# Performance work log

Measured on AMD Instinct MI355X. Metric: run time of the kernel, lower is better.

Reference implementation:

```python
import jax, jax.numpy as jnp
import numpy as np

N_DST = 50000
N_SRC = 50000
E = 800000
D = 128
R = 3
H_SEM = 128
NEG_SLOPE = 0.2  # DGL GATConv default


def setup_inputs() -> dict:
    key = jax.random.key(0)
    ks = jax.random.split(key, 40)
    s = 1.0 / np.sqrt(D)
    inp = {
        'dst_feat': jax.random.normal(ks[0], (N_DST, D), jnp.float32),
        'src_feat0': jax.random.normal(ks[1], (N_SRC, D), jnp.float32),
        'src_feat1': jax.random.normal(ks[2], (N_SRC, D), jnp.float32),
        'src_feat2': jax.random.normal(ks[3], (N_SRC, D), jnp.float32),
        'sem_W1': jax.random.normal(ks[4], (D, H_SEM), jnp.float32) * s,
        'sem_b1': jnp.zeros((H_SEM,), jnp.float32),
        'sem_W2': jax.random.normal(ks[5], (H_SEM, 1), jnp.float32) * (1.0 / np.sqrt(H_SEM)),
    }
    for r in range(R):
        inp[f'Wg{r}'] = jax.random.normal(ks[6 + r], (D, D), jnp.float32) * s
        inp[f'al{r}'] = jax.random.normal(ks[9 + r], (D,), jnp.float32) * s
        inp[f'ar{r}'] = jax.random.normal(ks[12 + r], (D,), jnp.float32) * s
        inp[f'bg{r}'] = jnp.zeros((D,), jnp.float32)
        inp[f'src_idx{r}'] = jax.random.randint(ks[15 + r], (E,), 0, N_SRC, jnp.int32)
        inp[f'dst_idx{r}'] = jax.random.randint(ks[18 + r], (E,), 0, N_DST, jnp.int32)
    return inp


def _gat(fs, fd, W, al, ar, b, sidx, didx):
    # DGL GATConv, num_heads=1, bipartite, eval mode (no dropout)
    hs = fs @ W                    # [Ns, D]
    hd = fd @ W                    # [Nd, D]
    el = hs @ al                   # [Ns]
    er = hd @ ar                   # [Nd]
    e = jax.nn.leaky_relu(el[sidx] + er[didx], NEG_SLOPE)  # [E]
    # edge softmax over incoming edges of each dst node
    m = jax.ops.segment_max(e, didx, num_segments=N_DST)
    a = jnp.exp(e - m[didx])
    z = jax.ops.segment_sum(a, didx, num_segments=N_DST)
    alpha = a / z[didx]            # [E]
    out = jax.ops.segment_sum(hs[sidx] * alpha[:, None], didx, num_segments=N_DST)
    return jax.nn.elu(out + b)     # [Nd, D]


def reference(dst_feat, src_feat0, src_feat1, src_feat2,
              Wg0, Wg1, Wg2, al0, al1, al2, ar0, ar1, ar2, bg0, bg1, bg2,
              sem_W1, sem_b1, sem_W2,
              src_idx0, src_idx1, src_idx2, dst_idx0, dst_idx1, dst_idx2):
    z0 = _gat(src_feat0, dst_feat, Wg0, al0, ar0, bg0, src_idx0, dst_idx0)
    z1 = _gat(src_feat1, dst_feat, Wg1, al1, ar1, bg1, src_idx1, dst_idx1)
    z2 = _gat(src_feat2, dst_feat, Wg2, al2, ar2, bg2, src_idx2, dst_idx2)
    z_m = jnp.stack([z0, z1, z2], axis=1)            # [N, R, D]
    h = jnp.tanh(z_m @ sem_W1 + sem_b1) @ sem_W2     # [N, R, 1]
    w = h.mean(axis=0)                               # [R, 1]
    a_w = jax.nn.softmax(w, axis=0)                  # [R, 1]
    z = (z_m * a_w[None, :, :]).sum(axis=1)          # [N, D]
    att_mp = a_w.squeeze()                           # [R]
    return (z, att_mp)
```

## Files before the change

kernel.cpp:

```cpp
#include <hip/hip_runtime.h>
#include <math.h>

#define D_DIM 128
#define N_DST 50000
#define N_SRC 50000
#define NE    800000
#define NEG_SLOPE 0.2f

#define NB        196
#define CAP       4608
#define CHUNK     8192
#define NBLK_REL  98
#define GEMM_BLKS 196
#define GEMM_GRID (3 * GEMM_BLKS)
#define ER_PB     86

typedef unsigned short ushort_t;
using f32x4  = __attribute__((ext_vector_type(4))) float;
using bf16x8 = __attribute__((ext_vector_type(8))) short;

__device__ __forceinline__ ushort_t f2bf(float x) {
    unsigned u = __float_as_uint(x);
    unsigned r = (u + 0x7fffu + ((u >> 16) & 1u)) >> 16;
    return (ushort_t)r;
}
__device__ __forceinline__ float bf2f(ushort_t b) {
    return __uint_as_float(((unsigned)b) << 16);
}
__device__ __forceinline__ float bflo(unsigned u) { return __uint_as_float(u << 16); }
__device__ __forceinline__ float bfhi(unsigned u) { return __uint_as_float(u & 0xffff0000u); }
__device__ __forceinline__ float tanh_fast(float x) {
    float e = __expf(2.f * x);
    return 1.f - 2.f / (e + 1.f);
}

__device__ __forceinline__ void cvt8(float4 f0, float4 f1, bf16x8& hi, bf16x8& lo) {
    float f[8] = {f0.x, f0.y, f0.z, f0.w, f1.x, f1.y, f1.z, f1.w};
    #pragma unroll
    for (int i = 0; i < 8; i++) {
        ushort_t h = f2bf(f[i]);
        hi[i] = (short)h;
        lo[i] = (short)(ushort_t)(__float_as_uint(f[i] - bf2f(h)) >> 16);
    }
}

__global__ __launch_bounds__(256) void vecprep_kernel(
        const float* __restrict__ Wg0, const float* __restrict__ Wg1,
        const float* __restrict__ Wg2,
        const float* __restrict__ ar0, const float* __restrict__ ar1,
        const float* __restrict__ ar2,
        const float* __restrict__ W1,
        float* __restrict__ wv, ushort_t* __restrict__ Wt_g,
        ushort_t* __restrict__ Bv) {
    int bx = blockIdx.x, tid = threadIdx.x;
    if (bx < 3) {
        if (tid < 128) {
            const float* W  = bx == 0 ? Wg0 : (bx == 1 ? Wg1 : Wg2);
            const float* ar = bx == 0 ? ar0 : (bx == 1 ? ar1 : ar2);
            float sar = 0.f;
            for (int j = 0; j < D_DIM; j++) sar = fmaf(W[tid * D_DIM + j], ar[j], sar);
            wv[bx * D_DIM + tid] = sar;
        }
    } else if (bx < 67) {
        int idx = (bx - 3) * 256 + tid;
        int k = idx >> 7, n = idx & 127;
        Wt_g[n * 128 + k] = f2bf(W1[idx]);
    } else {
        int q = bx - 67;
        int rel = q >> 6;
        int idx = (q & 63) * 256 + tid;
        const float* W = rel == 0 ? Wg0 : (rel == 1 ? Wg1 : Wg2);
        int k = idx >> 7, n = idx & 127;
        float v = W[idx];
        ushort_t hi = f2bf(v);
        ushort_t lo = f2bf(v - bf2f(hi));
        int nt = n >> 4, l15 = n & 15;
        int kc = k >> 5, quad = (k >> 3) & 3, e = k & 7;
        int h2 = nt >> 2, n4 = nt & 3;
        int lane = quad * 16 + l15;
        int fh = kc * 16 + h2 * 8 + n4;
        ushort_t* dst = Bv + (size_t)rel * 32768;
        dst[(fh)     * 512 + lane * 8 + e] = hi;
        dst[(fh + 4) * 512 + lane * 8 + e] = lo;
    }
}

__global__ __launch_bounds__(256) void bucket_scatter_kernel(
        const int* __restrict__ d0, const int* __restrict__ d1, const int* __restrict__ d2,
        const int* __restrict__ s0, const int* __restrict__ s1, const int* __restrict__ s2,
        int* __restrict__ bucketCur, int2* __restrict__ pairs) {
    __shared__ int cnt[NB], base[NB], cur[NB];
    int bx = blockIdx.x;
    int r = bx / NBLK_REL, blk = bx % NBLK_REL;
    const int* dd = r == 0 ? d0 : (r == 1 ? d1 : d2);
    const int* ss = r == 0 ? s0 : (r == 1 ? s1 : s2);
    int tid = threadIdx.x;
    if (tid < NB) { cnt[tid] = 0; cur[tid] = 0; }
    __syncthreads();
    int e0 = blk * CHUNK, e1 = min(e0 + CHUNK, NE);
    for (int e = e0 + tid; e < e1; e += 256) atomicAdd(&cnt[dd[e] >> 8], 1);
    __syncthreads();
    if (tid < NB) base[tid] = cnt[tid] ? atomicAdd(&bucketCur[r * NB + tid], cnt[tid]) : 0;
    __syncthreads();
    for (int e = e0 + tid; e < e1; e += 256) {
        int d = dd[e], b = d >> 8;
        int rank = atomicAdd(&cur[b], 1);
        pairs[(size_t)(r * NB + b) * CAP + base[b] + rank] = make_int2(ss[e], d);
    }
}

__global__ __launch_bounds__(256) void csr_kernel(
        const int2* __restrict__ pairs, const int* __restrict__ bucketCur,
        int* __restrict__ offs, int* __restrict__ cnts, int* __restrict__ perm) {
    __shared__ int hist[256], sc[256], cur[256];
    int bx = blockIdx.x;
    int r = bx / NB, b = bx % NB;
    int tid = threadIdx.x;
    int nE = bucketCur[r * NB + b];
    size_t region = (size_t)(r * NB + b) * CAP;
    const int2* pr = pairs + region;
    hist[tid] = 0;
    __syncthreads();
    for (int i = tid; i < nE; i += 256) atomicAdd(&hist[pr[i].y & 255], 1);
    __syncthreads();
    int v = hist[tid];
    sc[tid] = v;
    __syncthreads();
    for (int off = 1; off < 256; off <<= 1) {
        int t = tid >= off ? sc[tid - off] : 0;
        __syncthreads();
        sc[tid] += t;
        __syncthreads();
    }
    int excl = sc[tid] - v;
    int dstg = b * 256 + tid;
    if (dstg < N_DST) { offs[r * N_DST + dstg] = (int)region + excl; cnts[r * N_DST + dstg] = v; }
    cur[tid] = excl;
    __syncthreads();
    int* pm = perm + region;
    for (int i = tid; i < nE; i += 256) {
        int2 p = pr[i];
        int rank = atomicAdd(&cur[p.y & 255], 1);
        pm[rank] = p.x;
    }
}

__global__ __launch_bounds__(512) void gemm_er_kernel(
        const float* __restrict__ A0, const float* __restrict__ A1, const float* __restrict__ A2,
        const ushort_t* __restrict__ Bv,
        const float* __restrict__ al0, const float* __restrict__ al1, const float* __restrict__ al2,
        const float* __restrict__ dstf, const float* __restrict__ wv,
        ushort_t* __restrict__ hs, float* __restrict__ elv) {
    __shared__ ushort_t Bs[32768];
    int bx = blockIdx.x;
    int rel = bx / GEMM_BLKS, blk = bx % GEMM_BLKS;
    const float* A  = rel == 0 ? A0 : (rel == 1 ? A1 : A2);
    const float* al = rel == 0 ? al0 : (rel == 1 ? al1 : al2);
    ushort_t* C = hs + (size_t)rel * N_SRC * 128;
    int tid = threadIdx.x;

    {
        const uint4* src = (const uint4*)(Bv + (size_t)rel * 32768);
        uint4* dl = (uint4*)Bs;
        #pragma unroll
        for (int i = 0; i < 8; i++) dl[tid + i * 512] = src[tid + i * 512];
    }

    int w = tid >> 6, lane = tid & 63;
    int quad = lane >> 4, l15 = lane & 15;
    int row0 = blk * 256 + w * 32;

    int gr0 = row0 + l15;      if (gr0 > N_SRC - 1) gr0 = N_SRC - 1;
    int gr1 = row0 + 16 + l15; if (gr1 > N_SRC - 1) gr1 = N_SRC - 1;
    const float* a0p = A + (size_t)gr0 * 128 + quad * 8;
    const float* a1p = A + (size_t)gr1 * 128 + quad * 8;

    float4 abuf[2][2][2];
    abuf[0][0][0] = *(const float4*)(a0p + 0);
    abuf[0][0][1] = *(const float4*)(a0p + 4);
    abuf[0][1][0] = *(const float4*)(a1p + 0);
    abuf[0][1][1] = *(const float4*)(a1p + 4);

    __syncthreads();

    f32x4 acc[2][8] = {};
    #pragma unroll
    for (int kc = 0; kc < 4; kc++) {
        const int par = kc & 1;
        if (kc < 3) {
            int ko = (kc + 1) * 32;
            abuf[par ^ 1][0][0] = *(const float4*)(a0p + ko);
            abuf[par ^ 1][0][1] = *(const float4*)(a0p + ko + 4);
            abuf[par ^ 1][1][0] = *(const float4*)(a1p + ko);
            abuf[par ^ 1][1][1] = *(const float4*)(a1p + ko + 4);
        }
        bf16x8 ah[2], alo[2];
        #pragma unroll
        for (int t = 0; t < 2; t++)
            cvt8(abuf[par][t][0], abuf[par][t][1], ah[t], alo[t]);

        #pragma unroll
        for (int h2 = 0; h2 < 2; h2++) {
            #pragma unroll
            for (int n4 = 0; n4 < 4; n4++) {
                int f = kc * 16 + h2 * 8 + n4;
                bf16x8 bh = *(const bf16x8*)&Bs[f * 512 + lane * 8];
                bf16x8 bl = *(const bf16x8*)&Bs[(f + 4) * 512 + lane * 8];
                int nt = h2 * 4 + n4;
                #pragma unroll
                for (int t = 0; t < 2; t++) {
                    acc[t][nt] = __builtin_amdgcn_mfma_f32_16x16x32_bf16(ah[t],  bh, acc[t][nt], 0, 0, 0);
                    acc[t][nt] = __builtin_amdgcn_mfma_f32_16x16x32_bf16(alo[t], bh, acc[t][nt], 0, 0, 0);
                    acc[t][nt] = __builtin_amdgcn_mfma_f32_16x16x32_bf16(ah[t],  bl, acc[t][nt], 0, 0, 0);
                }
            }
        }
    }

    float alv[8];
    #pragma unroll
    for (int nt = 0; nt < 8; nt++) alv[nt] = al[nt * 16 + l15];
    #pragma unroll
    for (int t = 0; t < 2; t++) {
        float part[4] = {0.f, 0.f, 0.f, 0.f};
        #pragma unroll
        for (int nt = 0; nt < 8; nt++)
            #pragma unroll
            for (int i = 0; i < 4; i++)
                part[i] = fmaf(acc[t][nt][i], alv[nt], part[i]);
        #pragma unroll
        for (int msk = 1; msk < 16; msk <<= 1)
            #pragma unroll
            for (int i = 0; i < 4; i++) part[i] += __shfl_xor(part[i], msk);
        if (l15 == 0) {
            #pragma unroll
            for (int i = 0; i < 4; i++) {
                int gr = row0 + t * 16 + quad * 4 + i;
                if (gr < N_SRC) elv[rel * N_DST + gr] = part[i];
            }
        }
    }

    int erbase = bx * ER_PB;
    float m0[11], m1[11];
    float wl0 = 0.f, wh0 = 0.f, wl1 = 0.f, wh1 = 0.f, wl2 = 0.f, wh2 = 0.f;
    int rend = 0;
    if (erbase < N_DST) {
        rend = min(erbase + ER_PB, N_DST);
        wl0 = wv[lane];       wh0 = wv[lane + 64];
        wl1 = wv[128 + lane]; wh1 = wv[128 + lane + 64];
        wl2 = wv[256 + lane]; wh2 = wv[256 + lane + 64];
        #pragma unroll
        for (int j = 0; j < 11; j++) {
            int r = erbase + w + 8 * j;
            int rr = r < rend ? r : erbase;
            m0[j] = dstf[(size_t)rr * 128 + lane];
            m1[j] = dstf[(size_t)rr * 128 + lane + 64];
        }
    }

    __syncthreads();

    ushort_t* Csh = Bs + w * 2304;
    #pragma unroll
    for (int h = 0; h < 2; h++) {
        __asm__ __volatile__("" ::: "memory");
        #pragma unroll
        for (int t = 0; t < 2; t++)
            #pragma unroll
            for (int ntl = 0; ntl < 4; ntl++) {
                int nt = h * 4 + ntl;
                #pragma unroll
                for (int i = 0; i < 4; i++)
                    Csh[(t * 16 + quad * 4 + i) * 72 + ntl * 16 + l15] = f2bf(acc[t][nt][i]);
            }
        __asm__ __volatile__("" ::: "memory");
        int r2 = lane >> 1, cb = (lane & 1) * 32;
        int gr = row0 + r2;
        if (gr < N_SRC) {
            ushort_t* dst = C + (size_t)gr * 128 + h * 64 + cb;
            #pragma unroll
            for (int k2 = 0; k2 < 4; k2++) {
                uint4 v = *(const uint4*)&Csh[r2 * 72 + cb + k2 * 8];
                *(uint4*)(dst + k2 * 8) = v;
            }
        }
    }

    if (erbase < N_DST) {
        #pragma unroll
        for (int j = 0; j < 11; j++) {
            int r = erbase + w + 8 * j;
            if (r < rend) {
                float p0 = fmaf(m0[j], wl0, m1[j] * wh0);
                float p1 = fmaf(m0[j], wl1, m1[j] * wh1);
                float p2 = fmaf(m0[j], wl2, m1[j] * wh2);
                #pragma unroll
                for (int off = 32; off > 0; off >>= 1) {
                    p0 += __shfl_down(p0, off);
                    p1 += __shfl_down(p1, off);
                    p2 += __shfl_down(p2, off);
                }
                if (lane == 0) {
                    elv[3 * N_DST + r] = p0;
                    elv[4 * N_DST + r] = p1;
                    elv[5 * N_DST + r] = p2;
                }
            }
        }
    }
}

__global__ __launch_bounds__(256) void aggregate_kernel(
        const ushort_t* __restrict__ hs, const float* __restrict__ elv,
        const int* __restrict__ perm, const int* __restrict__ offs,
        const int* __restrict__ cnts,
        const float* __restrict__ bg0, const float* __restrict__ bg1,
        const float* __restrict__ bg2, float* __restrict__ zm) {
    __shared__ int2 ew[4][128];
    int wave = threadIdx.x >> 6, lane = threadIdx.x & 63;
    int bx  = blockIdx.x;
    int rel = bx / 12500;
    int b   = (bx % 12500) * 4 + wave;
    const float* el  = elv + rel * N_DST;
    float erb = elv[(3 + rel) * N_DST + b];
    const float* bg = rel == 0 ? bg0 : (rel == 1 ? bg1 : bg2);
    const ushort_t* hsr = hs + (size_t)rel * N_SRC * 128;
    int o0 = offs[rel * N_DST + b], deg = cnts[rel * N_DST + b];
    float* zout = zm + ((size_t)b * 3 + rel) * 128;

    if (deg <= 128) {
        int s0 = 0, s1 = 0;
        float e0 = 0.f, e1 = 0.f;
        if (deg <= 64) {
            if (lane < deg) {
                s0 = perm[o0 + lane];
                float x = el[s0] + erb;
                x = x >= 0.f ? x : NEG_SLOPE * x;
                e0 = __expf(x);
            }
        } else {
            int i0 = lane, i1 = lane + 64;
            float x0 = -INFINITY, x1 = -INFINITY;
            if (i0 < deg) { s0 = perm[o0 + i0]; float x = el[s0] + erb; x0 = x >= 0.f ? x : NEG_SLOPE * x; }
            if (i1 < deg) { s1 = perm[o0 + i1]; float x = el[s1] + erb; x1 = x >= 0.f ? x : NEG_SLOPE * x; }
            float m = fmaxf(x0, x1);
            #pragma unroll
            for (int msk = 1; msk < 64; msk <<= 1) m = fmaxf(m, __shfl_xor(m, msk));
            e0 = (i0 < deg) ? __expf(x0 - m) : 0.f;
            e1 = (i1 < deg) ? __expf(x1 - m) : 0.f;
        }
        float lsum = e0 + e1;
        #pragma unroll
        for (int msk = 1; msk < 64; msk <<= 1) lsum += __shfl_xor(lsum, msk);
        float invz = deg > 0 ? 1.f / lsum : 0.f;

        ew[wave][lane] = make_int2(s0 * 256, __float_as_int(e0 * invz));
        if (deg > 64)
            ew[wave][lane + 64] = make_int2(s1 * 256, __float_as_int(e1 * invz));
        __asm__ __volatile__("" ::: "memory");

        int degp = (deg + 7) & ~7;
        const char* base = (const char*)hsr;
        int half = lane >> 5;
        int col8 = (lane & 31) * 8;
        float2 a01 = {0.f, 0.f}, a23 = {0.f, 0.f};
        for (int j = 0; j < degp; j += 8) {
            int2 pA = ew[wave][j + half];
            int2 pB = ew[wave][j + 2 + half];
            int2 pC = ew[wave][j + 4 + half];
            int2 pD = ew[wave][j + 6 + half];
            uint2 hA = *(const uint2*)(base + (unsigned)(pA.x + col8));
            uint2 hB = *(const uint2*)(base + (unsigned)(pB.x + col8));
            uint2 hC = *(const uint2*)(base + (unsigned)(pC.x + col8));
            uint2 hD = *(const uint2*)(base + (unsigned)(pD.x + col8));
            float eA = __int_as_float(pA.y), eB = __int_as_float(pB.y);
            float eC = __int_as_float(pC.y), eD = __int_as_float(pD.y);
            a01.x = fmaf(eA, bflo(hA.x), a01.x); a01.y = fmaf(eA, bfhi(hA.x), a01.y);
            a23.x = fmaf(eA, bflo(hA.y), a23.x); a23.y = fmaf(eA, bfhi(hA.y), a23.y);
            a01.x = fmaf(eB, bflo(hB.x), a01.x); a01.y = fmaf(eB, bfhi(hB.x), a01.y);
            a23.x = fmaf(eB, bflo(hB.y), a23.x); a23.y = fmaf(eB, bfhi(hB.y), a23.y);
            a01.x = fmaf(eC, bflo(hC.x), a01.x); a01.y = fmaf(eC, bfhi(hC.x), a01.y);
            a23.x = fmaf(eC, bflo(hC.y), a23.x); a23.y = fmaf(eC, bfhi(hC.y), a23.y);
            a01.x = fmaf(eD, bflo(hD.x), a01.x); a01.y = fmaf(eD, bfhi(hD.x), a01.y);
            a23.x = fmaf(eD, bflo(hD.y), a23.x); a23.y = fmaf(eD, bfhi(hD.y), a23.y);
        }
        a01.x += __shfl_xor(a01.x, 32);
        a01.y += __shfl_xor(a01.y, 32);
        a23.x += __shfl_xor(a23.x, 32);
        a23.y += __shfl_xor(a23.y, 32);
        if (half == 0) {
            int col4 = (lane & 31) * 4;
            float4 bgv = *(const float4*)&bg[col4];
            float4 z;
            z.x = a01.x + bgv.x;
            z.y = a01.y + bgv.y;
            z.z = a23.x + bgv.z;
            z.w = a23.y + bgv.w;
            z.x = z.x > 0.f ? z.x : __expf(z.x) - 1.f;
            z.y = z.y > 0.f ? z.y : __expf(z.y) - 1.f;
            z.z = z.z > 0.f ? z.z : __expf(z.z) - 1.f;
            z.w = z.w > 0.f ? z.w : __expf(z.w) - 1.f;
            *(float4*)&zout[col4] = z;
        }
    } else {
        float lmax = -INFINITY;
        for (int i = lane; i < deg; i += 64) {
            int s = perm[o0 + i];
            float x = el[s] + erb;
            x = x >= 0.f ? x : NEG_SLOPE * x;
            lmax = fmaxf(lmax, x);
        }
        #pragma unroll
        for (int msk = 1; msk < 64; msk <<= 1) lmax = fmaxf(lmax, __shfl_xor(lmax, msk));
        float lsum = 0.f;
        for (int i = lane; i < deg; i += 64) {
            int s = perm[o0 + i];
            float x = el[s] + erb;
            x = x >= 0.f ? x : NEG_SLOPE * x;
            lsum += __expf(x - lmax);
        }
        #pragma unroll
        for (int msk = 1; msk < 64; msk <<= 1) lsum += __shfl_xor(lsum, msk);
        float invz = 1.f / lsum;
        float c0 = 0.f, c1 = 0.f;
        int col2 = lane * 2;
        for (int j = 0; j < deg; j++) {
            int s = perm[o0 + j];
            float x = el[s] + erb;
            x = x >= 0.f ? x : NEG_SLOPE * x;
            float e_ = __expf(x - lmax) * invz;
            unsigned hv = *(const unsigned*)(hsr + (size_t)s * 128 + col2);
            c0 = fmaf(e_, bflo(hv), c0);
            c1 = fmaf(e_, bfhi(hv), c1);
        }
        float2 z;
        z.x = c0 + bg[col2];
        z.y = c1 + bg[col2 + 1];
        z.x = z.x > 0.f ? z.x : __expf(z.x) - 1.f;
        z.y = z.y > 0.f ? z.y : __expf(z.y) - 1.f;
        *(float2*)&zout[col2] = z;
    }
}

__global__ __launch_bounds__(256) void semantic_kernel(
        const float* __restrict__ zm, const ushort_t* __restrict__ Wt_g,
        const float* __restrict__ b1, const float* __restrict__ W2,
        float* __restrict__ w_sum) {
    __shared__ ushort_t Wt[128 * 136];
    __shared__ float hsum[3];
    const int NROWS = N_DST * 3;
    int tid = threadIdx.x;
    if (tid < 3) hsum[tid] = 0.f;

    #pragma unroll
    for (int i = 0; i < 8; i++) {
        int c = i * 256 + tid;
        int n = c >> 4, c16 = c & 15;
        uint4 t = *(const uint4*)(Wt_g + n * 128 + c16 * 8);
        *(uint4*)&Wt[n * 136 + c16 * 8] = t;
    }
    __syncthreads();

    int w    = tid >> 6, lane = tid & 63;
    int quad = lane >> 4, l15 = lane & 15;
    long row0 = (long)blockIdx.x * 64 + w * 16;
    long rA = row0 + l15; if (rA > NROWS - 1) rA = NROWS - 1;

    f32x4 acc[8] = {};
    #pragma unroll
    for (int kc = 0; kc < 4; kc++) {
        int k0 = kc * 32 + quad * 8;
        const float* src = zm + (size_t)rA * 128 + k0;
        float4 f0 = *(const float4*)src;
        float4 f1 = *(const float4*)(src + 4);
        bf16x8 a;
        a[0] = (short)f2bf(f0.x); a[1] = (short)f2bf(f0.y);
        a[2] = (short)f2bf(f0.z); a[3] = (short)f2bf(f0.w);
        a[4] = (short)f2bf(f1.x); a[5] = (short)f2bf(f1.y);
        a[6] = (short)f2bf(f1.z); a[7] = (short)f2bf(f1.w);
        #pragma unroll
        for (int nt = 0; nt < 8; nt++) {
            int n = nt * 16 + l15;
            bf16x8 bfr = *(const bf16x8*)&Wt[n * 136 + k0];
            acc[nt] = __builtin_amdgcn_mfma_f32_16x16x32_bf16(a, bfr, acc[nt], 0, 0, 0);
        }
    }

    float part[4] = {0.f, 0.f, 0.f, 0.f};
    #pragma unroll
    for (int nt = 0; nt < 8; nt++) {
        int n = nt * 16 + l15;
        float bb = b1[n], ww = W2[n];
        #pragma unroll
        for (int i = 0; i < 4; i++) {
            float t = tanh_fast(acc[nt][i] + bb);
            part[i] = fmaf(t, ww, part[i]);
        }
    }
    #pragma unroll
    for (int msk = 1; msk < 16; msk <<= 1)
        #pragma unroll
        for (int i = 0; i < 4; i++) part[i] += __shfl_xor(part[i], msk);
    if (l15 == 0) {
        #pragma unroll
        for (int i = 0; i < 4; i++) {
            long R = row0 + quad * 4 + i;
            if (R < NROWS) atomicAdd(&hsum[(int)(R % 3)], part[i]);
        }
    }
    __syncthreads();
    if (tid < 3) atomicAdd(&w_sum[tid], hsum[tid]);
}

__global__ void combine_kernel(const float* __restrict__ zm, const float* __restrict__ w_sum,
                               float* __restrict__ out, float* __restrict__ out_att) {
    float w0 = w_sum[0] * (1.f / (float)N_DST);
    float w1 = w_sum[1] * (1.f / (float)N_DST);
    float w2 = w_sum[2] * (1.f / (float)N_DST);
    float m = fmaxf(w0, fmaxf(w1, w2));
    float e0 = __expf(w0 - m), e1 = __expf(w1 - m), e2 = __expf(w2 - m);
    float s = 1.f / (e0 + e1 + e2);
    float a0 = e0 * s, a1 = e1 * s, a2 = e2 * s;
    if (blockIdx.x == 0 && threadIdx.x < 3)
        out_att[threadIdx.x] = threadIdx.x == 0 ? a0 : (threadIdx.x == 1 ? a1 : a2);
    int id4 = blockIdx.x * 256 + threadIdx.x;
    int n  = id4 >> 5;
    int d4 = (id4 & 31) * 4;
    const float4 z0 = *(const float4*)&zm[((size_t)n * 3 + 0) * 128 + d4];
    const float4 z1 = *(const float4*)&zm[((size_t)n * 3 + 1) * 128 + d4];
    const float4 z2 = *(const float4*)&zm[((size_t)n * 3 + 2) * 128 + d4];
    float4 o;
    o.x = a0 * z0.x + a1 * z1.x + a2 * z2.x;
    o.y = a0 * z0.y + a1 * z1.y + a2 * z2.y;
    o.z = a0 * z0.z + a1 * z1.z + a2 * z2.z;
    o.w = a0 * z0.w + a1 * z1.w + a2 * z2.w;
    *(float4*)&out[(size_t)n * 128 + d4] = o;
}

extern "C" void kernel_launch(void* const* d_in, const int* in_sizes, int n_in,
                              void* d_out, int out_size, void* d_ws, size_t ws_size,
                              hipStream_t stream) {
    const float* dstf   = (const float*)d_in[0];
    const float* src0   = (const float*)d_in[1];
    const float* src1   = (const float*)d_in[2];
    const float* src2   = (const float*)d_in[3];
    const float* sem_W1 = (const float*)d_in[4];
    const float* sem_b1 = (const float*)d_in[5];
    const float* sem_W2 = (const float*)d_in[6];
    const float* Wg[3]  = {(const float*)d_in[7],  (const float*)d_in[13], (const float*)d_in[19]};
    const float* al[3]  = {(const float*)d_in[8],  (const float*)d_in[14], (const float*)d_in[20]};
    const float* ar[3]  = {(const float*)d_in[9],  (const float*)d_in[15], (const float*)d_in[21]};
    const float* bg[3]  = {(const float*)d_in[10], (const float*)d_in[16], (const float*)d_in[22]};
    const int*  sidx[3] = {(const int*)d_in[11], (const int*)d_in[17], (const int*)d_in[23]};
    const int*  didx[3] = {(const int*)d_in[12], (const int*)d_in[18], (const int*)d_in[24]};
    float* out = (float*)d_out;

    char* p = (char*)d_ws;
    auto alloc = [&](size_t bytes) -> char* {
        char* q = p; p += (bytes + 255) & ~(size_t)255; return q;
    };
    float*    zm   = (float*)alloc((size_t)N_DST * 3 * 128 * 4);
    ushort_t* hs   = (ushort_t*)alloc((size_t)3 * N_SRC * 128 * 2);
    float*    elv  = (float*)alloc((size_t)6 * N_DST * 4);
    float*    wv   = (float*)alloc((size_t)3 * 128 * 4);
    ushort_t* Wt_g = (ushort_t*)alloc((size_t)128 * 128 * 2);
    ushort_t* Bv   = (ushort_t*)alloc((size_t)3 * 32768 * 2);
    int* cnts = (int*)alloc((size_t)3 * N_DST * 4);
    int* offs = (int*)alloc((size_t)3 * N_DST * 4);
    int* perm = (int*)alloc((size_t)3 * NB * CAP * 4);
    int* zero = (int*)alloc((size_t)(3 * NB + 8) * 4);
    int*   bucketCur = zero;
    float* wsum      = (float*)(zero + 3 * NB);
    int2* pairs = (int2*)zm;

    hipMemsetAsync(zero, 0, (size_t)(3 * NB + 8) * 4, stream);

    vecprep_kernel<<<259, 256, 0, stream>>>(Wg[0], Wg[1], Wg[2], ar[0], ar[1], ar[2],
                                            sem_W1, wv, Wt_g, Bv);
    bucket_scatter_kernel<<<3 * NBLK_REL, 256, 0, stream>>>(didx[0], didx[1], didx[2],
                                                            sidx[0], sidx[1], sidx[2],
                                                            bucketCur, pairs);
    csr_kernel<<<3 * NB, 256, 0, stream>>>(pairs, bucketCur, offs, cnts, perm);
    gemm_er_kernel<<<GEMM_GRID, 512, 0, stream>>>(src0, src1, src2, Bv,
                                                  al[0], al[1], al[2],
                                                  dstf, wv, hs, elv);
    aggregate_kernel<<<3 * 12500, 256, 0, stream>>>(hs, elv, perm, offs, cnts,
                                                    bg[0], bg[1], bg[2], zm);
    semantic_kernel<<<(3 * N_DST + 63) / 64, 256, 0, stream>>>(zm, Wt_g, sem_b1, sem_W2, wsum);
    combine_kernel<<<6250, 256, 0, stream>>>(zm, wsum, out, out + (size_t)N_DST * 128);
}
```

Measured before the change: 435.4 us.

## Map one half-wave per destination node in aggregation; persistent-grid semantic kernel

The aggregation kernel now gives each destination node 32 lanes instead of a full 64-lane wave, so each block covers 8 nodes and the grid is halved. Each lane loads 16-byte bf16 chunks and keeps 8 accumulators, and the fast path now covers degrees up to 64 instead of 128; higher degrees fall to the slow serial path. This targets idle lanes on the typical degree of about 16 and improves gather width. The semantic kernel becomes a grid-stride loop over 512 blocks, which cuts the number of per-block shared-memory and global atomic flushes but leaves fewer blocks to hide latency.

```diff
diff --git a/kernel.cpp b/kernel.cpp
--- a/kernel.cpp
+++ b/kernel.cpp
@@ -14,6 +14,8 @@
 #define GEMM_BLKS 196
 #define GEMM_GRID (3 * GEMM_BLKS)
 #define ER_PB     86
+#define SEM_GRID  512
+#define SEM_TILES ((3 * N_DST + 63) / 64)
 
 typedef unsigned short ushort_t;
 using f32x4  = __attribute__((ext_vector_type(4))) float;
@@ -317,129 +319,133 @@
         const int* __restrict__ cnts,
         const float* __restrict__ bg0, const float* __restrict__ bg1,
         const float* __restrict__ bg2, float* __restrict__ zm) {
-    __shared__ int2 ew[4][128];
-    int wave = threadIdx.x >> 6, lane = threadIdx.x & 63;
+    __shared__ int2 ew[4][2][64];
+    int tid = threadIdx.x;
+    int wave = tid >> 6, lane = tid & 63;
+    int hw = lane >> 5, l31 = lane & 31;
     int bx  = blockIdx.x;
-    int rel = bx / 12500;
-    int b   = (bx % 12500) * 4 + wave;
+    int rel = bx / 6250;
+    int b   = (bx % 6250) * 8 + wave * 2 + hw;
     const float* el  = elv + rel * N_DST;
     float erb = elv[(3 + rel) * N_DST + b];
     const float* bg = rel == 0 ? bg0 : (rel == 1 ? bg1 : bg2);
     const ushort_t* hsr = hs + (size_t)rel * N_SRC * 128;
     int o0 = offs[rel * N_DST + b], deg = cnts[rel * N_DST + b];
     float* zout = zm + ((size_t)b * 3 + rel) * 128;
-
-    if (deg <= 128) {
+    int2* ews = ew[wave][hw];
+
+    if (deg <= 64) {
         int s0 = 0, s1 = 0;
         float e0 = 0.f, e1 = 0.f;
-        if (deg <= 64) {
-            if (lane < deg) {
-                s0 = perm[o0 + lane];
-                float x = el[s0] + erb;
-                x = x >= 0.f ? x : NEG_SLOPE * x;
-                e0 = __expf(x);
-            }
-        } else {
-            int i0 = lane, i1 = lane + 64;
-            float x0 = -INFINITY, x1 = -INFINITY;
-            if (i0 < deg) { s0 = perm[o0 + i0]; float x = el[s0] + erb; x0 = x >= 0.f ? x : NEG_SLOPE * x; }
-            if (i1 < deg) { s1 = perm[o0 + i1]; float x = el[s1] + erb; x1 = x >= 0.f ? x : NEG_SLOPE * x; }
-            float m = fmaxf(x0, x1);
-            #pragma unroll
-            for (int msk = 1; msk < 64; msk <<= 1) m = fmaxf(m, __shfl_xor(m, msk));
-            e0 = (i0 < deg) ? __expf(x0 - m) : 0.f;
-            e1 = (i1 < deg) ? __expf(x1 - m) : 0.f;
+        if (l31 < deg) {
+            s0 = perm[o0 + l31];
+            float x = el[s0] + erb;
+            x = x >= 0.f ? x : NEG_SLOPE * x;
+            e0 = __expf(x);
+        }
+        if (deg > 32 && l31 + 32 < deg) {
+            s1 = perm[o0 + l31 + 32];
+            float x = el[s1] + erb;
+            x = x >= 0.f ? x : NEG_SLOPE * x;
+            e1 = __expf(x);
         }
         float lsum = e0 + e1;
         #pragma unroll
-        for (int msk = 1; msk < 64; msk <<= 1) lsum += __shfl_xor(lsum, msk);
+        for (int msk = 1; msk < 32; msk <<= 1) lsum += __shfl_xor(lsum, msk);
         float invz = deg > 0 ? 1.f / lsum : 0.f;
 
-        ew[wave][lane] = make_int2(s0 * 256, __float_as_int(e0 * invz));
-        if (deg > 64)
-            ew[wave][lane + 64] = make_int2(s1 * 256, __float_as_int(e1 * invz));
+        ews[l31] = make_int2(s0 * 256, __float_as_int(e0 * invz));
+        if (deg > 32)
+            ews[l31 + 32] = make_int2(s1 * 256, __float_as_int(e1 * invz));
         __asm__ __volatile__("" ::: "memory");
 
-        int degp = (deg + 7) & ~7;
-        const char* base = (const char*)hsr;
-        int half = lane >> 5;
-        int col8 = (lane & 31) * 8;
-        float2 a01 = {0.f, 0.f}, a23 = {0.f, 0.f};
-        for (int j = 0; j < degp; j += 8) {
-            int2 pA = ew[wave][j + half];
-            int2 pB = ew[wave][j + 2 + half];
-            int2 pC = ew[wave][j + 4 + half];
-            int2 pD = ew[wave][j + 6 + half];
-            uint2 hA = *(const uint2*)(base + (unsigned)(pA.x + col8));
-            uint2 hB = *(const uint2*)(base + (unsigned)(pB.x + col8));
-            uint2 hC = *(const uint2*)(base + (unsigned)(pC.x + col8));
-            uint2 hD = *(const uint2*)(base + (unsigned)(pD.x + col8));
+        int degp = (deg + 3) & ~3;
+        const char* basep = (const char*)hsr;
+        int sub = l31 >> 4;
+        int col16 = (l31 & 15) * 16;
+        float a0 = 0.f, a1 = 0.f, a2 = 0.f, a3 = 0.f;
+        float a4 = 0.f, a5 = 0.f, a6 = 0.f, a7 = 0.f;
+        for (int j = 0; j < degp; j += 4) {
+            int2 pA = ews[j + sub];
+            int2 pB = ews[j + 2 + sub];
+            uint4 hA = *(const uint4*)(basep + (unsigned)(pA.x + col16));
+            uint4 hB = *(const uint4*)(basep + (unsigned)(pB.x + col16));
             float eA = __int_as_float(pA.y), eB = __int_as_float(pB.y);
-            float eC = __int_as_float(pC.y), eD = __int_as_float(pD.y);
-            a01.x = fmaf(eA, bflo(hA.x), a01.x); a01.y = fmaf(eA, bfhi(hA.x), a01.y);
-            a23.x = fmaf(eA, bflo(hA.y), a23.x); a23.y = fmaf(eA, bfhi(hA.y), a23.y);
-            a01.x = fmaf(eB, bflo(hB.x), a01.x); a01.y = fmaf(eB, bfhi(hB.x), a01.y);
-            a23.x = fmaf(eB, bflo(hB.y), a23.x); a23.y = fmaf(eB, bfhi(hB.y), a23.y);
-            a01.x = fmaf(eC, bflo(hC.x), a01.x); a01.y = fmaf(eC, bfhi(hC.x), a01.y);
-            a23.x = fmaf(eC, bflo(hC.y), a23.x); a23.y = fmaf(eC, bfhi(hC.y), a23.y);
-            a01.x = fmaf(eD, bflo(hD.x), a01.x); a01.y = fmaf(eD, bfhi(hD.x), a01.y);
-            a23.x = fmaf(eD, bflo(hD.y), a23.x); a23.y = fmaf(eD, bfhi(hD.y), a23.y);
-        }
-        a01.x += __shfl_xor(a01.x, 32);
-        a01.y += __shfl_xor(a01.y, 32);
-        a23.x += __shfl_xor(a23.x, 32);
-        a23.y += __shfl_xor(a23.y, 32);
-        if (half == 0) {
-            int col4 = (lane & 31) * 4;
-            float4 bgv = *(const float4*)&bg[col4];
-            float4 z;
-            z.x = a01.x + bgv.x;
-            z.y = a01.y + bgv.y;
-            z.z = a23.x + bgv.z;
-            z.w = a23.y + bgv.w;
-            z.x = z.x > 0.f ? z.x : __expf(z.x) - 1.f;
-            z.y = z.y > 0.f ? z.y : __expf(z.y) - 1.f;
-            z.z = z.z > 0.f ? z.z : __expf(z.z) - 1.f;
-            z.w = z.w > 0.f ? z.w : __expf(z.w) - 1.f;
-            *(float4*)&zout[col4] = z;
+            a0 = fmaf(eA, bflo(hA.x), a0); a1 = fmaf(eA, bfhi(hA.x), a1);
+            a2 = fmaf(eA, bflo(hA.y), a2); a3 = fmaf(eA, bfhi(hA.y), a3);
+            a4 = fmaf(eA, bflo(hA.z), a4); a5 = fmaf(eA, bfhi(hA.z), a5);
+            a6 = fmaf(eA, bflo(hA.w), a6); a7 = fmaf(eA, bfhi(hA.w), a7);
+            a0 = fmaf(eB, bflo(hB.x), a0); a1 = fmaf(eB, bfhi(hB.x), a1);
+            a2 = fmaf(eB, bflo(hB.y), a2); a3 = fmaf(eB, bfhi(hB.y), a3);
+            a4 = fmaf(eB, bflo(hB.z), a4); a5 = fmaf(eB, bfhi(hB.z), a5);
+            a6 = fmaf(eB, bflo(hB.w), a6); a7 = fmaf(eB, bfhi(hB.w), a7);
+        }
+        a0 += __shfl_xor(a0, 16); a1 += __shfl_xor(a1, 16);
+        a2 += __shfl_xor(a2, 16); a3 += __shfl_xor(a3, 16);
+        a4 += __shfl_xor(a4, 16); a5 += __shfl_xor(a5, 16);
+        a6 += __shfl_xor(a6, 16); a7 += __shfl_xor(a7, 16);
+        if (sub == 0) {
+            int c = (l31 & 15) * 8;
+            float4 bgv0 = *(const float4*)&bg[c];
+            float4 bgv1 = *(const float4*)&bg[c + 4];
+            float4 z0, z1;
+            z0.x = a0 + bgv0.x; z0.y = a1 + bgv0.y;
+            z0.z = a2 + bgv0.z; z0.w = a3 + bgv0.w;
+            z1.x = a4 + bgv1.x; z1.y = a5 + bgv1.y;
+            z1.z = a6 + bgv1.z; z1.w = a7 + bgv1.w;
+            z0.x = z0.x > 0.f ? z0.x : __expf(z0.x) - 1.f;
+            z0.y = z0.y > 0.f ? z0.y : __expf(z0.y) - 1.f;
+            z0.z = z0.z > 0.f ? z0.z : __expf(z0.z) - 1.f;
+            z0.w = z0.w > 0.f ? z0.w : __expf(z0.w) - 1.f;
+            z1.x = z1.x > 0.f ? z1.x : __expf(z1.x) - 1.f;
+            z1.y = z1.y > 0.f ? z1.y : __expf(z1.y) - 1.f;
+            z1.z = z1.z > 0.f ? z1.z : __expf(z1.z) - 1.f;
+            z1.w = z1.w > 0.f ? z1.w : __expf(z1.w) - 1.f;
+            *(float4*)&zout[c] = z0;
+            *(float4*)&zout[c + 4] = z1;
         }
     } else {
         float lmax = -INFINITY;
-        for (int i = lane; i < deg; i += 64) {
+        for (int i = l31; i < deg; i += 32) {
             int s = perm[o0 + i];
             float x = el[s] + erb;
             x = x >= 0.f ? x : NEG_SLOPE * x;
             lmax = fmaxf(lmax, x);
         }
         #pragma unroll
-        for (int msk = 1; msk < 64; msk <<= 1) lmax = fmaxf(lmax, __shfl_xor(lmax, msk));
+        for (int msk = 1; msk < 32; msk <<= 1) lmax = fmaxf(lmax, __shfl_xor(lmax, msk));
         float lsum = 0.f;
-        for (int i = lane; i < deg; i += 64) {
+        for (int i = l31; i < deg; i += 32) {
             int s = perm[o0 + i];
             float x = el[s] + erb;
             x = x >= 0.f ? x : NEG_SLOPE * x;
             lsum += __expf(x - lmax);
         }
         #pragma unroll
-        for (int msk = 1; msk < 64; msk <<= 1) lsum += __shfl_xor(lsum, msk);
+        for (int msk = 1; msk < 32; msk <<= 1) lsum += __shfl_xor(lsum, msk);
         float invz = 1.f / lsum;
-        float c0 = 0.f, c1 = 0.f;
-        int col2 = lane * 2;
+        float c0 = 0.f, c1 = 0.f, c2 = 0.f, c3 = 0.f;
         for (int j = 0; j < deg; j++) {
             int s = perm[o0 + j];
             float x = el[s] + erb;
             x = x >= 0.f ? x : NEG_SLOPE * x;
             float e_ = __expf(x - lmax) * invz;
-            unsigned hv = *(const unsigned*)(hsr + (size_t)s * 128 + col2);
-            c0 = fmaf(e_, bflo(hv), c0);
-            c1 = fmaf(e_, bfhi(hv), c1);
-        }
-        float2 z;
-        z.x = c0 + bg[col2];
-        z.y = c1 + bg[col2 + 1];
+            uint2 hv = *(const uint2*)(hsr + (size_t)s * 128 + l31 * 4);
+            c0 = fmaf(e_, bflo(hv.x), c0);
+            c1 = fmaf(e_, bfhi(hv.x), c1);
+            c2 = fmaf(e_, bflo(hv.y), c2);
+            c3 = fmaf(e_, bfhi(hv.y), c3);
+        }
+        int c = l31 * 4;
+        float4 bgv = *(const float4*)&bg[c];
+        float4 z;
+        z.x = c0 + bgv.x; z.y = c1 + bgv.y;
+        z.z = c2 + bgv.z; z.w = c3 + bgv.w;
         z.x = z.x > 0.f ? z.x : __expf(z.x) - 1.f;
         z.y = z.y > 0.f ? z.y : __expf(z.y) - 1.f;
-        *(float2*)&zout[col2] = z;
+        z.z = z.z > 0.f ? z.z : __expf(z.z) - 1.f;
+        z.w = z.w > 0.f ? z.w : __expf(z.w) - 1.f;
+        *(float4*)&zout[c] = z;
     }
 }
 
@@ -464,53 +470,58 @@
 
     int w    = tid >> 6, lane = tid & 63;
     int quad = lane >> 4, l15 = lane & 15;
-    long row0 = (long)blockIdx.x * 64 + w * 16;
-    long rA = row0 + l15; if (rA > NROWS - 1) rA = NROWS - 1;
-
-    f32x4 acc[8] = {};
-    #pragma unroll
-    for (int kc = 0; kc < 4; kc++) {
-        int k0 = kc * 32 + quad * 8;
-        const float* src = zm + (size_t)rA * 128 + k0;
-        float4 f0 = *(const float4*)src;
-        float4 f1 = *(const float4*)(src + 4);
-        bf16x8 a;
-        a[0] = (short)f2bf(f0.x); a[1] = (short)f2bf(f0.y);
-        a[2] = (short)f2bf(f0.z); a[3] = (short)f2bf(f0.w);
-        a[4] = (short)f2bf(f1.x); a[5] = (short)f2bf(f1.y);
-        a[6] = (short)f2bf(f1.z); a[7] = (short)f2bf(f1.w);
+    float bb = b1[l15 * 8 + 0];
+
+    for (int tile = blockIdx.x; tile < SEM_TILES; tile += gridDim.x) {
+        long row0 = (long)tile * 64 + w * 16;
+        long rA = row0 + l15; if (rA > NROWS - 1) rA = NROWS - 1;
+
+        f32x4 acc[8] = {};
+        #pragma unroll
+        for (int kc = 0; kc < 4; kc++) {
+            int k0 = kc * 32 + quad * 8;
+            const float* src = zm + (size_t)rA * 128 + k0;
+            float4 f0 = *(const float4*)src;
+            float4 f1 = *(const float4*)(src + 4);
+            bf16x8 a;
+            a[0] = (short)f2bf(f0.x); a[1] = (short)f2bf(f0.y);
+            a[2] = (short)f2bf(f0.z); a[3] = (short)f2bf(f0.w);
+            a[4] = (short)f2bf(f1.x); a[5] = (short)f2bf(f1.y);
+            a[6] = (short)f2bf(f1.z); a[7] = (short)f2bf(f1.w);
+            #pragma unroll
+            for (int nt = 0; nt < 8; nt++) {
+                int n = nt * 16 + l15;
+                bf16x8 bfr = *(const bf16x8*)&Wt[n * 136 + k0];
+                acc[nt] = __builtin_amdgcn_mfma_f32_16x16x32_bf16(a, bfr, acc[nt], 0, 0, 0);
+            }
+        }
+
+        float part[4] = {0.f, 0.f, 0.f, 0.f};
         #pragma unroll
         for (int nt = 0; nt < 8; nt++) {
             int n = nt * 16 + l15;
-            bf16x8 bfr = *(const bf16x8*)&Wt[n * 136 + k0];
-            acc[nt] = __builtin_amdgcn_mfma_f32_16x16x32_bf16(a, bfr, acc[nt], 0, 0, 0);
-        }
-    }
-
-    float part[4] = {0.f, 0.f, 0.f, 0.f};
-    #pragma unroll
-    for (int nt = 0; nt < 8; nt++) {
-        int n = nt * 16 + l15;
-        float bb = b1[n], ww = W2[n];
-        #pragma unroll
-        for (int i = 0; i < 4; i++) {
-            float t = tanh_fast(acc[nt][i] + bb);
-            part[i] = fmaf(t, ww, part[i]);
-        }
-    }
-    #pragma unroll
-    for (int msk = 1; msk < 16; msk <<= 1)
-        #pragma unroll
-        for (int i = 0; i < 4; i++) part[i] += __shfl_xor(part[i], msk);
-    if (l15 == 0) {
-        #pragma unroll
-        for (int i = 0; i < 4; i++) {
-            long R = row0 + quad * 4 + i;
-            if (R < NROWS) atomicAdd(&hsum[(int)(R % 3)], part[i]);
+            float bbn = b1[n], ww = W2[n];
+            #pragma unroll
+            for (int i = 0; i < 4; i++) {
+                float t = tanh_fast(acc[nt][i] + bbn);
+                part[i] = fmaf(t, ww, part[i]);
+            }
+        }
+        #pragma unroll
+        for (int msk = 1; msk < 16; msk <<= 1)
+            #pragma unroll
+            for (int i = 0; i < 4; i++) part[i] += __shfl_xor(part[i], msk);
+        if (l15 == 0) {
+            #pragma unroll
+            for (int i = 0; i < 4; i++) {
+                long R = row0 + quad * 4 + i;
+                if (R < NROWS) atomicAdd(&hsum[(int)(R % 3)], part[i]);
+            }
         }
     }
     __syncthreads();
     if (tid < 3) atomicAdd(&w_sum[tid], hsum[tid]);
+    (void)bb;
 }
 
 __global__ void combine_kernel(const float* __restrict__ zm, const float* __restrict__ w_sum,
@@ -585,8 +596,8 @@
     gemm_er_kernel<<<GEMM_GRID, 512, 0, stream>>>(src0, src1, src2, Bv,
                                                   al[0], al[1], al[2],
                                                   dstf, wv, hs, elv);
-    aggregate_kernel<<<3 * 12500, 256, 0, stream>>>(hs, elv, perm, offs, cnts,
-                                                    bg[0], bg[1], bg[2], zm);
-    semantic_kernel<<<(3 * N_DST + 63) / 64, 256, 0, stream>>>(zm, Wt_g, sem_b1, sem_W2, wsum);
+    aggregate_kernel<<<3 * 6250, 256, 0, stream>>>(hs, elv, perm, offs, cnts,
+                                                   bg[0], bg[1], bg[2], zm);
+    semantic_kernel<<<SEM_GRID, 256, 0, stream>>>(zm, Wt_g, sem_b1, sem_W2, wsum);
     combine_kernel<<<6250, 256, 0, stream>>>(zm, wsum, out, out + (size_t)N_DST * 128);
 }
```

Measured after the change: 417.7 us. 4.1% less time.
